# Kernel optimization log

Measured on AMD Instinct MI355X. Metric: run time of the kernel, lower is better.

## Reference

```python
import jax, jax.numpy as jnp
import numpy as np

B, S, D, H = 4, 2048, 768, 12
DEPTH = D // H


def setup_inputs() -> dict:
    key = jax.random.key(0)
    ks = jax.random.split(key, 8)
    scale = 1.0 / np.sqrt(D)
    inp = {
        "q": jax.random.normal(ks[0], (B, S, D), jnp.float32),
        "k": jax.random.normal(ks[1], (B, S, D), jnp.float32),
        "v": jax.random.normal(ks[2], (B, S, D), jnp.float32),
        # additive mask: 1.0 at disallowed (future) positions, causal
        "mask": jnp.triu(jnp.ones((S, S), jnp.float32), k=1)[None, None, :, :],
        "wq": jax.random.normal(ks[3], (D, D), jnp.float32) * scale,
        "wk": jax.random.normal(ks[4], (D, D), jnp.float32) * scale,
        "wv": jax.random.normal(ks[5], (D, D), jnp.float32) * scale,
        "w_dense": jax.random.normal(ks[6], (D, D), jnp.float32) * scale,
        "b_dense": jnp.zeros((D,), jnp.float32),
    }
    return inp


def _split_heads(x):
    b, s, _ = x.shape
    return x.reshape(b, s, H, DEPTH).transpose(0, 2, 1, 3)  # [B,H,S,depth]


def reference(q, k, v, mask, wq, wk, wv, w_dense, b_dense):
    qh = _split_heads(q @ wq.T)
    kh = _split_heads(k @ wk.T)
    vh = _split_heads(v @ wv.T)
    scale = jnp.sqrt(jnp.float32(DEPTH))
    logits = jnp.einsum("bhqd,bhkd->bhqk", qh, kh) / scale  # [B,H,S,S]
    logits = logits + mask * -1e9
    attn = jax.nn.softmax(logits, axis=-1)
    out = jnp.einsum("bhqk,bhkd->bhqd", attn, vh)
    out = out.transpose(0, 2, 1, 3).reshape(q.shape[0], -1, D)
    return out @ w_dense.T + b_dense
```

## Files before the change

kernel.cpp:

```cpp
#include <hip/hip_runtime.h>

typedef __attribute__((ext_vector_type(8))) short short8;
typedef __attribute__((ext_vector_type(4))) float f32x4;
typedef __attribute__((ext_vector_type(4))) unsigned int uint4v;

static __device__ __forceinline__ unsigned pack2(float x, float y) {
  unsigned ux = __float_as_uint(x) + 0x8000u;
  unsigned uy = __float_as_uint(y) + 0x8000u;
  return __builtin_amdgcn_perm(uy, ux, 0x07060302u);
}
static __device__ __forceinline__ unsigned packt(float x, float y) {
  return __builtin_amdgcn_perm(__float_as_uint(y), __float_as_uint(x), 0x07060302u);
}

#define GLDS(g, l)                                                                     \
  __builtin_amdgcn_global_load_lds((const __attribute__((address_space(1))) void*)(g), \
                                   (__attribute__((address_space(3))) void*)(l), 16, 0, 0)

__global__ __launch_bounds__(256) void cvt_all(const float* __restrict__ q,
                                               const float* __restrict__ k,
                                               const float* __restrict__ v,
                                               const float* __restrict__ w0,
                                               const float* __restrict__ w1,
                                               const float* __restrict__ w2,
                                               const float* __restrict__ w3,
                                               unsigned short* __restrict__ oq,
                                               unsigned short* __restrict__ ok,
                                               unsigned short* __restrict__ ov,
                                               unsigned short* __restrict__ o0,
                                               unsigned short* __restrict__ o1,
                                               unsigned short* __restrict__ o2,
                                               unsigned short* __restrict__ o3) {
  const int bx = blockIdx.x;
  const float* s;
  unsigned short* d;
  long i;
  if (bx < 18432) {
    int seg = bx / 6144;
    s = seg == 0 ? q : seg == 1 ? k : v;
    d = seg == 0 ? oq : seg == 1 ? ok : ov;
    i = (long)(bx - seg * 6144) * 256 + threadIdx.x;
  } else {
    int t = bx - 18432;
    int seg = t / 576;
    s = seg == 0 ? w0 : seg == 1 ? w1 : seg == 2 ? w2 : w3;
    d = seg == 0 ? o0 : seg == 1 ? o1 : seg == 2 ? o2 : o3;
    i = (long)(t - seg * 576) * 256 + threadIdx.x;
  }
  float4 val = ((const float4*)s)[i];
  uint2 o;
  o.x = pack2(val.x, val.y);
  o.y = pack2(val.z, val.w);
  *(uint2*)(d + 4 * i) = o;
}

template <int MODE>
static __device__ __forceinline__ void proj_body(const unsigned short* __restrict__ A,
                                                 const unsigned short* __restrict__ W,
                                                 unsigned short* __restrict__ O, int m0,
                                                 int n0, unsigned short* buf) {
  constexpr int K = 768;
  const int tid = threadIdx.x, lane = tid & 63, wave = tid >> 6;
  const int ln = lane & 15, quad = lane >> 4;
  const int wm = (wave & 1) << 6, wn = (wave >> 1) << 6;

  const int o0 = tid << 4, o1 = 4096 + (tid << 4);
  const unsigned short* gA0 = A + (long)(m0 + (o0 >> 6)) * K + ((o0 >> 4) & 3) * 8;
  const unsigned short* gA1 = A + (long)(m0 + (o1 >> 6)) * K + ((o1 >> 4) & 3) * 8;
  const unsigned short* gW0 = W + (long)(n0 + (o0 >> 6)) * K + ((o0 >> 4) & 3) * 8;
  const unsigned short* gW1 = W + (long)(n0 + (o1 >> 6)) * K + ((o1 >> 4) & 3) * 8;

  GLDS(gA0, buf + (o0 >> 1));
  GLDS(gA1, buf + (o1 >> 1));
  GLDS(gW0, buf + 8192 + (o0 >> 1));
  GLDS(gW1, buf + 8192 + (o1 >> 1));

  f32x4 acc[4][4] = {};
  for (int t = 0; t < 24; t++) {
    const int cur = t & 1, nxt = cur ^ 1;
    const int k1 = (t + 1) << 5;
    __syncthreads();
    if (t < 23) {
      GLDS(gA0 + k1, buf + nxt * 4096 + (o0 >> 1));
      GLDS(gA1 + k1, buf + nxt * 4096 + (o1 >> 1));
      GLDS(gW0 + k1, buf + 8192 + nxt * 4096 + (o0 >> 1));
      GLDS(gW1 + k1, buf + 8192 + nxt * 4096 + (o1 >> 1));
    }
    const unsigned short* As = buf + cur * 4096;
    const unsigned short* Bs = buf + 8192 + cur * 4096;
    short8 af[4], bfr[4];
#pragma unroll
    for (int mi = 0; mi < 4; mi++)
      af[mi] = *(const short8*)(As + (wm + mi * 16 + ln) * 32 + quad * 8);
#pragma unroll
    for (int ni = 0; ni < 4; ni++)
      bfr[ni] = *(const short8*)(Bs + (wn + ni * 16 + ln) * 32 + quad * 8);
#pragma unroll
    for (int mi = 0; mi < 4; mi++)
#pragma unroll
      for (int ni = 0; ni < 4; ni++)
        acc[mi][ni] = (MODE == 0)
                          ? __builtin_amdgcn_mfma_f32_16x16x32_bf16(bfr[ni], af[mi],
                                                                    acc[mi][ni], 0, 0, 0)
                          : __builtin_amdgcn_mfma_f32_16x16x32_bf16(af[mi], bfr[ni],
                                                                    acc[mi][ni], 0, 0, 0);
  }

  unsigned short* Ts = buf;
  __syncthreads();
  if (MODE == 0) {
#pragma unroll
    for (int mi = 0; mi < 4; mi++)
#pragma unroll
      for (int ni = 0; ni < 4; ni++) {
        f32x4 v = acc[mi][ni];
        int s = wm + mi * 16 + ln;
        int n = wn + ni * 16 + quad * 4;
        uint2 w2;
        w2.x = pack2(v[0], v[1]);
        w2.y = pack2(v[2], v[3]);
        *(uint2*)(Ts + s * 136 + n) = w2;
      }
    __syncthreads();
    const int part = tid & 7, sg0 = tid >> 3;
#pragma unroll
    for (int p = 0; p < 8; p++) {
      int seg = sg0 + p * 32;
      int hh = seg >> 7, s = seg & 127;
      short8 val = *(const short8*)(Ts + s * 136 + hh * 64 + part * 8);
      int gs = m0 + s;
      int bb = gs >> 11, srow = gs & 2047;
      int head = (n0 >> 6) + hh;
      *(short8*)(O + (((long)(bb * 12 + head) * 2048 + srow) << 6) + part * 8) = val;
    }
  } else {
#pragma unroll
    for (int mi = 0; mi < 4; mi++)
#pragma unroll
      for (int ni = 0; ni < 4; ni++) {
        f32x4 v = acc[mi][ni];
        int d = wn + ni * 16 + ln;
        int s = wm + mi * 16 + quad * 4;
        uint2 w2;
        w2.x = pack2(v[0], v[1]);
        w2.y = pack2(v[2], v[3]);
        *(uint2*)(Ts + d * 136 + s) = w2;
      }
    __syncthreads();
    const int part = tid & 15, r0 = tid >> 4;
    const int bb = m0 >> 11, sbase = m0 & 2047;
#pragma unroll
    for (int p = 0; p < 8; p++) {
      int d = r0 + p * 16;
      short8 val = *(const short8*)(Ts + d * 136 + part * 8);
      int head = (n0 >> 6) + (d >> 6);
      int dl = d & 63;
      *(short8*)(O + ((long)(bb * 12 + head) * 64 + dl) * 2048 + sbase + part * 8) = val;
    }
  }
}

__global__ __launch_bounds__(256) void proj_all(
    const unsigned short* __restrict__ qb, const unsigned short* __restrict__ kb,
    const unsigned short* __restrict__ vb, const unsigned short* __restrict__ wq,
    const unsigned short* __restrict__ wk, const unsigned short* __restrict__ wv,
    unsigned short* __restrict__ qh, unsigned short* __restrict__ kh,
    unsigned short* __restrict__ vt) {
  __shared__ unsigned short buf[17408];
  const int bx = blockIdx.x;
  const int xcd = bx & 7;
  const int i = bx >> 3;
  const int op = i / 48, j = i % 48;
  const int m0 = ((j / 6) * 8 + xcd) << 7, n0 = (j % 6) << 7;
  if (op == 0)
    proj_body<0>(qb, wq, qh, m0, n0, buf);
  else if (op == 1)
    proj_body<0>(kb, wk, kh, m0, n0, buf);
  else
    proj_body<1>(vb, wv, vt, m0, n0, buf);
}

__global__ __launch_bounds__(256) void dense_gemm(const unsigned short* __restrict__ A,
                                                  const unsigned short* __restrict__ W,
                                                  const float* __restrict__ bias,
                                                  float* __restrict__ out) {
  constexpr int K = 768;
  __shared__ unsigned short buf[16384];
  const int bx = blockIdx.x;
  const int xcd = bx & 7;
  const int i = bx >> 3;
  const int m0 = ((i / 6) * 8 + xcd) << 7;
  const int n0 = (i % 6) << 7;

  const int tid = threadIdx.x, lane = tid & 63, wave = tid >> 6;
  const int ln = lane & 15, quad = lane >> 4;
  const int wm = (wave & 1) << 6, wn = (wave >> 1) << 6;

  const int o0 = tid << 4, o1 = 4096 + (tid << 4);
  const unsigned short* gA0 = A + (long)(m0 + (o0 >> 6)) * K + ((o0 >> 4) & 3) * 8;
  const unsigned short* gA1 = A + (long)(m0 + (o1 >> 6)) * K + ((o1 >> 4) & 3) * 8;
  const unsigned short* gW0 = W + (long)(n0 + (o0 >> 6)) * K + ((o0 >> 4) & 3) * 8;
  const unsigned short* gW1 = W + (long)(n0 + (o1 >> 6)) * K + ((o1 >> 4) & 3) * 8;

  GLDS(gA0, buf + (o0 >> 1));
  GLDS(gA1, buf + (o1 >> 1));
  GLDS(gW0, buf + 8192 + (o0 >> 1));
  GLDS(gW1, buf + 8192 + (o1 >> 1));

  f32x4 acc[4][4] = {};
  for (int t = 0; t < 24; t++) {
    const int cur = t & 1, nxt = cur ^ 1;
    const int k1 = (t + 1) << 5;
    __syncthreads();
    if (t < 23) {
      GLDS(gA0 + k1, buf + nxt * 4096 + (o0 >> 1));
      GLDS(gA1 + k1, buf + nxt * 4096 + (o1 >> 1));
      GLDS(gW0 + k1, buf + 8192 + nxt * 4096 + (o0 >> 1));
      GLDS(gW1 + k1, buf + 8192 + nxt * 4096 + (o1 >> 1));
    }
    const unsigned short* As = buf + cur * 4096;
    const unsigned short* Bs = buf + 8192 + cur * 4096;
    short8 af[4], bfr[4];
#pragma unroll
    for (int mi = 0; mi < 4; mi++)
      af[mi] = *(const short8*)(As + (wm + mi * 16 + ln) * 32 + quad * 8);
#pragma unroll
    for (int ni = 0; ni < 4; ni++)
      bfr[ni] = *(const short8*)(Bs + (wn + ni * 16 + ln) * 32 + quad * 8);
#pragma unroll
    for (int mi = 0; mi < 4; mi++)
#pragma unroll
      for (int ni = 0; ni < 4; ni++)
        acc[mi][ni] =
            __builtin_amdgcn_mfma_f32_16x16x32_bf16(bfr[ni], af[mi], acc[mi][ni], 0, 0, 0);
  }

#pragma unroll
  for (int mi = 0; mi < 4; mi++) {
    const int m = m0 + wm + mi * 16 + ln;
#pragma unroll
    for (int ni = 0; ni < 4; ni++) {
      const int n = n0 + wn + ni * 16 + quad * 4;
      f32x4 v = acc[mi][ni];
      float4 bv = *(const float4*)(bias + n);
      float4 st;
      st.x = v[0] + bv.x;
      st.y = v[1] + bv.y;
      st.z = v[2] + bv.z;
      st.w = v[3] + bv.w;
      *(float4*)(out + (long)m * 768 + n) = st;
    }
  }
}

__global__ __launch_bounds__(256, 3) void attn_kernel(const unsigned short* __restrict__ Qh,
                                                      const unsigned short* __restrict__ Kh,
                                                      const unsigned short* __restrict__ Vt,
                                                      unsigned short* __restrict__ outp) {
  constexpr int S = 2048;
  constexpr float CEXP = 0.18033688011112042f;
  __shared__ unsigned short sbuf[16384];

  const int bx = blockIdx.x;
  const int xcd = bx & 7;
  const int ii = bx >> 3;
  const int pr = ii & 15, grp = ii >> 4;
  const int bh = grp * 8 + xcd;
  const int h = bh % 12, b = bh / 12;
  const int qtA = pr, qtB = 31 - pr;
  const int tid = threadIdx.x, wave = tid >> 6, lane = tid & 63;
  const int ln = lane & 15, quad = lane >> 4;

  const unsigned short* Qg = Qh + (long)(b * 12 + h) * S * 64;
  const unsigned short* Kg = Kh + (long)(b * 12 + h) * S * 64;
  const unsigned short* Vg = Vt + (long)(b * 12 + h) * 64 * S;

  const int qrA = qtA * 64 + wave * 16 + ln;
  const int qrB = qtB * 64 + wave * 16 + ln;

  short8 bQa0 = *(const short8*)(Qg + qrA * 64 + quad * 8);
  short8 bQa1 = *(const short8*)(Qg + qrA * 64 + 32 + quad * 8);
  short8 bQb0 = *(const short8*)(Qg + qrB * 64 + quad * 8);
  short8 bQb1 = *(const short8*)(Qg + qrB * 64 + 32 + quad * 8);

  float sumA = 0.f, sumB = 0.f;
  f32x4 Oa[4] = {};
  f32x4 Ob[4] = {};
  unsigned pkA[8][2], pkB[8][2];

  const int nkA = (qtA >> 1) + 1;
  const int nkB = (qtB >> 1) + 1;
  const int l0 = ln + ((quad & 1) << 5);
  const bool hi = quad >= 2;

  const int srow = tid >> 2, sc = (tid & 3) << 3;
  const int koff0 = srow * 64 + sc;
  const int koff1 = (srow + 64) * 64 + sc;
  const int koff2 = srow * 64 + 32 + sc;
  const int koff3 = (srow + 64) * 64 + 32 + sc;
  const long voff = (long)srow * 2048 + sc;

  short8 kc[4], vc[4];
  {
    kc[0] = *(const short8*)(Kg + koff0);
    kc[1] = *(const short8*)(Kg + koff1);
    kc[2] = *(const short8*)(Kg + koff2);
    kc[3] = *(const short8*)(Kg + koff3);
    vc[0] = *(const short8*)(Vg + voff);
    vc[1] = *(const short8*)(Vg + voff + 32);
    vc[2] = *(const short8*)(Vg + voff + 64);
    vc[3] = *(const short8*)(Vg + voff + 96);
  }

  for (int kt = 0; kt < nkB; kt++) {
    __syncthreads();
    {
      unsigned short* w = sbuf + tid * 8;
      *(short8*)(w) = kc[0];
      *(short8*)(w + 2048) = kc[1];
      *(short8*)(w + 4096) = kc[2];
      *(short8*)(w + 6144) = kc[3];
      *(short8*)(w + 8192) = vc[0];
      *(short8*)(w + 10240) = vc[1];
      *(short8*)(w + 12288) = vc[2];
      *(short8*)(w + 14336) = vc[3];
    }
    __syncthreads();
    if (kt + 1 < nkB) {
      const unsigned short* kg = Kg + (kt + 1) * 8192;
      const unsigned short* vg = Vg + (kt + 1) * 128;
      kc[0] = *(const short8*)(kg + koff0);
      kc[1] = *(const short8*)(kg + koff1);
      kc[2] = *(const short8*)(kg + koff2);
      kc[3] = *(const short8*)(kg + koff3);
      vc[0] = *(const short8*)(vg + voff);
      vc[1] = *(const short8*)(vg + voff + 32);
      vc[2] = *(const short8*)(vg + voff + 64);
      vc[3] = *(const short8*)(vg + voff + 96);
    }

    const bool actA = kt < nkA;
    const bool dgA = actA && (kt == nkA - 1);
    const bool dgB = (kt == nkB - 1);
    const int limA = actA ? (dgA ? ((qtA & 1) ? 8 : 4) : 8) : 0;
    const int limB = dgB ? ((qtB & 1) ? 8 : 4) : 8;
    const int limQ = limA > limB ? limA : limB;
    const int kbase = kt * 128 + quad * 4;

#pragma unroll
    for (int ni = 0; ni < 8; ni++) {
      if (ni < limQ) {
        const int fro = (ni * 16 + ln) * 32 + quad * 8;
        short8 k0 = *(const short8*)(sbuf + fro);
        short8 k1 = *(const short8*)(sbuf + 4096 + fro);
        const int key = kbase + ni * 16;
        if (ni < limA) {
          f32x4 s = {};
          s = __builtin_amdgcn_mfma_f32_16x16x32_bf16(k0, bQa0, s, 0, 0, 0);
          s = __builtin_amdgcn_mfma_f32_16x16x32_bf16(k1, bQa1, s, 0, 0, 0);
          float p0 = exp2f(s[0] * CEXP), p1 = exp2f(s[1] * CEXP);
          float p2 = exp2f(s[2] * CEXP), p3 = exp2f(s[3] * CEXP);
          if (dgA) {
            p0 = (key + 0 > qrA) ? 0.f : p0;
            p1 = (key + 1 > qrA) ? 0.f : p1;
            p2 = (key + 2 > qrA) ? 0.f : p2;
            p3 = (key + 3 > qrA) ? 0.f : p3;
          }
          sumA += (p0 + p1) + (p2 + p3);
          pkA[ni][0] = packt(p0, p1);
          pkA[ni][1] = packt(p2, p3);
        }
        if (ni < limB) {
          f32x4 s = {};
          s = __builtin_amdgcn_mfma_f32_16x16x32_bf16(k0, bQb0, s, 0, 0, 0);
          s = __builtin_amdgcn_mfma_f32_16x16x32_bf16(k1, bQb1, s, 0, 0, 0);
          float p0 = exp2f(s[0] * CEXP), p1 = exp2f(s[1] * CEXP);
          float p2 = exp2f(s[2] * CEXP), p3 = exp2f(s[3] * CEXP);
          if (dgB) {
            p0 = (key + 0 > qrB) ? 0.f : p0;
            p1 = (key + 1 > qrB) ? 0.f : p1;
            p2 = (key + 2 > qrB) ? 0.f : p2;
            p3 = (key + 3 > qrB) ? 0.f : p3;
          }
          sumB += (p0 + p1) + (p2 + p3);
          pkB[ni][0] = packt(p0, p1);
          pkB[ni][1] = packt(p2, p3);
        }
      }
    }

    auto mkB = [&](unsigned (&pk)[8][2], int kk) -> short8 {
      unsigned va0 = (unsigned)__shfl((int)pk[2 * kk][0], l0, 64);
      unsigned vb0 = (unsigned)__shfl((int)pk[2 * kk + 1][0], l0, 64);
      unsigned va1 = (unsigned)__shfl((int)pk[2 * kk][1], l0, 64);
      unsigned vb1 = (unsigned)__shfl((int)pk[2 * kk + 1][1], l0, 64);
      unsigned va2 = (unsigned)__shfl((int)pk[2 * kk][0], l0 + 16, 64);
      unsigned vb2 = (unsigned)__shfl((int)pk[2 * kk + 1][0], l0 + 16, 64);
      unsigned va3 = (unsigned)__shfl((int)pk[2 * kk][1], l0 + 16, 64);
      unsigned vb3 = (unsigned)__shfl((int)pk[2 * kk + 1][1], l0 + 16, 64);
      uint4v tv;
      tv.x = hi ? vb0 : va0;
      tv.y = hi ? vb1 : va1;
      tv.z = hi ? vb2 : va2;
      tv.w = hi ? vb3 : va3;
      return __builtin_bit_cast(short8, tv);
    };

    const int kkA = limA >> 1, kkB = limB >> 1;
#pragma unroll
    for (int kk = 0; kk < 4; kk++) {
      if (kk < kkB) {
        short8 Bb = mkB(pkB, kk);
        short8 Ba;
        if (kk < kkA) Ba = mkB(pkA, kk);
        const unsigned short* vp = sbuf + 8192 + kk * 2048;
#pragma unroll
        for (int di = 0; di < 4; di++) {
          short8 aV = *(const short8*)(vp + (di * 16 + ln) * 32 + quad * 8);
          Ob[di] = __builtin_amdgcn_mfma_f32_16x16x32_bf16(aV, Bb, Ob[di], 0, 0, 0);
          if (kk < kkA) Oa[di] = __builtin_amdgcn_mfma_f32_16x16x32_bf16(aV, Ba, Oa[di], 0, 0, 0);
        }
      }
    }
  }

  sumA += __shfl_xor(sumA, 16);
  sumA += __shfl_xor(sumA, 32);
  sumB += __shfl_xor(sumB, 16);
  sumB += __shfl_xor(sumB, 32);

  __syncthreads();
  unsigned short* Ts = sbuf;
  {
    float rlA = 1.0f / sumA, rlB = 1.0f / sumB;
    const int row = wave * 16 + ln;
#pragma unroll
    for (int di = 0; di < 4; di++) {
      uint2 wa, wb;
      wa.x = pack2(Oa[di][0] * rlA, Oa[di][1] * rlA);
      wa.y = pack2(Oa[di][2] * rlA, Oa[di][3] * rlA);
      wb.x = pack2(Ob[di][0] * rlB, Ob[di][1] * rlB);
      wb.y = pack2(Ob[di][2] * rlB, Ob[di][3] * rlB);
      *(uint2*)(Ts + row * 72 + di * 16 + quad * 4) = wa;
      *(uint2*)(Ts + (row + 64) * 72 + di * 16 + quad * 4) = wb;
    }
  }
  __syncthreads();
  const int part = tid & 7, r0 = tid >> 3;
#pragma unroll
  for (int p = 0; p < 4; p++) {
    int row = r0 + p * 32;
    int seg = row >> 6, qq = row & 63;
    int qrow = (seg ? qtB : qtA) * 64 + qq;
    short8 val = *(const short8*)(Ts + row * 72 + part * 8);
    *(short8*)(outp + ((long)b * S + qrow) * 768 + h * 64 + part * 8) = val;
  }
}

extern "C" void kernel_launch(void* const* d_in, const int* in_sizes, int n_in,
                              void* d_out, int out_size, void* d_ws, size_t ws_size,
                              hipStream_t stream) {
  const float* q = (const float*)d_in[0];
  const float* k = (const float*)d_in[1];
  const float* v = (const float*)d_in[2];
  const float* wq = (const float*)d_in[4];
  const float* wk = (const float*)d_in[5];
  const float* wv = (const float*)d_in[6];
  const float* wd = (const float*)d_in[7];
  const float* bd = (const float*)d_in[8];
  float* out = (float*)d_out;

  const long QKV = 4L * 2048 * 768;
  const long WN = 768L * 768;
  if (ws_size < (size_t)(7 * QKV + 4 * WN) * 2) return;

  unsigned short* qb = (unsigned short*)d_ws;
  unsigned short* kb = qb + QKV;
  unsigned short* vb = kb + QKV;
  unsigned short* wqb = vb + QKV;
  unsigned short* wkb = wqb + WN;
  unsigned short* wvb = wkb + WN;
  unsigned short* wdb = wvb + WN;
  unsigned short* qh = wdb + WN;
  unsigned short* kh = qh + QKV;
  unsigned short* vt = kh + QKV;
  unsigned short* at = vt + QKV;

  cvt_all<<<20736, 256, 0, stream>>>(q, k, v, wq, wk, wv, wd, qb, kb, vb, wqb, wkb, wvb, wdb);
  proj_all<<<1152, 256, 0, stream>>>(qb, kb, vb, wqb, wkb, wvb, qh, kh, vt);
  attn_kernel<<<768, 256, 0, stream>>>(qh, kh, vt, at);
  dense_gemm<<<384, 256, 0, stream>>>(at, wdb, bd, out);
}
```

Before: 271.2 us.

## Fuse fp32-to-bf16 activation conversion into projection GEMM and fold softmax scale into Q

The projection GEMM now streams the fp32 q/k/v activations straight into LDS with an XOR-swizzled layout and packs them to bf16 while loading fragments. This removes the separate conversion pass over the large activations and its bf16 round trip through global memory, leaving only a small weight-conversion kernel. The softmax exponent scale is applied to Q in the projection epilogue, so the attention inner loop drops a multiply per score. In exchange the A tile doubles in LDS size and global traffic, and each fragment load does extra packing ALU work.

```diff
diff --git a/kernel.cpp b/kernel.cpp
--- a/kernel.cpp
+++ b/kernel.cpp
@@ -17,36 +17,20 @@
   __builtin_amdgcn_global_load_lds((const __attribute__((address_space(1))) void*)(g), \
                                    (__attribute__((address_space(3))) void*)(l), 16, 0, 0)
 
-__global__ __launch_bounds__(256) void cvt_all(const float* __restrict__ q,
-                                               const float* __restrict__ k,
-                                               const float* __restrict__ v,
-                                               const float* __restrict__ w0,
-                                               const float* __restrict__ w1,
-                                               const float* __restrict__ w2,
-                                               const float* __restrict__ w3,
-                                               unsigned short* __restrict__ oq,
-                                               unsigned short* __restrict__ ok,
-                                               unsigned short* __restrict__ ov,
-                                               unsigned short* __restrict__ o0,
-                                               unsigned short* __restrict__ o1,
-                                               unsigned short* __restrict__ o2,
-                                               unsigned short* __restrict__ o3) {
-  const int bx = blockIdx.x;
-  const float* s;
-  unsigned short* d;
-  long i;
-  if (bx < 18432) {
-    int seg = bx / 6144;
-    s = seg == 0 ? q : seg == 1 ? k : v;
-    d = seg == 0 ? oq : seg == 1 ? ok : ov;
-    i = (long)(bx - seg * 6144) * 256 + threadIdx.x;
-  } else {
-    int t = bx - 18432;
-    int seg = t / 576;
-    s = seg == 0 ? w0 : seg == 1 ? w1 : seg == 2 ? w2 : w3;
-    d = seg == 0 ? o0 : seg == 1 ? o1 : seg == 2 ? o2 : o3;
-    i = (long)(t - seg * 576) * 256 + threadIdx.x;
-  }
+__global__ __launch_bounds__(256) void cvt_w(const float* __restrict__ w0,
+                                             const float* __restrict__ w1,
+                                             const float* __restrict__ w2,
+                                             const float* __restrict__ w3,
+                                             unsigned short* __restrict__ o0,
+                                             unsigned short* __restrict__ o1,
+                                             unsigned short* __restrict__ o2,
+                                             unsigned short* __restrict__ o3) {
+  int bx = blockIdx.x;
+  int seg = bx / 576;
+  int t = bx - seg * 576;
+  const float* s = seg == 0 ? w0 : seg == 1 ? w1 : seg == 2 ? w2 : w3;
+  unsigned short* d = seg == 0 ? o0 : seg == 1 ? o1 : seg == 2 ? o2 : o3;
+  long i = (long)t * 256 + threadIdx.x;
   float4 val = ((const float4*)s)[i];
   uint2 o;
   o.x = pack2(val.x, val.y);
@@ -55,25 +39,44 @@
 }
 
 template <int MODE>
-static __device__ __forceinline__ void proj_body(const unsigned short* __restrict__ A,
+static __device__ __forceinline__ void proj_body(const float* __restrict__ A,
                                                  const unsigned short* __restrict__ W,
                                                  unsigned short* __restrict__ O, int m0,
-                                                 int n0, unsigned short* buf) {
+                                                 int n0, unsigned short* buf, float scale) {
   constexpr int K = 768;
+  float* Af = (float*)buf;
+  unsigned short* Wb = buf + 16384;
   const int tid = threadIdx.x, lane = tid & 63, wave = tid >> 6;
   const int ln = lane & 15, quad = lane >> 4;
   const int wm = (wave & 1) << 6, wn = (wave >> 1) << 6;
 
+  const float* gA[4];
+  float* lA[4];
+#pragma unroll
+  for (int i = 0; i < 4; i++) {
+    int s = tid + i * 256;
+    int row = s >> 3;
+    int cg = (s & 7) ^ (row & 7);
+    gA[i] = A + (long)(m0 + row) * K + cg * 4;
+    lA[i] = Af + s * 4;
+  }
   const int o0 = tid << 4, o1 = 4096 + (tid << 4);
-  const unsigned short* gA0 = A + (long)(m0 + (o0 >> 6)) * K + ((o0 >> 4) & 3) * 8;
-  const unsigned short* gA1 = A + (long)(m0 + (o1 >> 6)) * K + ((o1 >> 4) & 3) * 8;
   const unsigned short* gW0 = W + (long)(n0 + (o0 >> 6)) * K + ((o0 >> 4) & 3) * 8;
   const unsigned short* gW1 = W + (long)(n0 + (o1 >> 6)) * K + ((o1 >> 4) & 3) * 8;
 
-  GLDS(gA0, buf + (o0 >> 1));
-  GLDS(gA1, buf + (o1 >> 1));
-  GLDS(gW0, buf + 8192 + (o0 >> 1));
-  GLDS(gW1, buf + 8192 + (o1 >> 1));
+  int fpo[4][2];
+#pragma unroll
+  for (int mi = 0; mi < 4; mi++) {
+    int R = wm + mi * 16 + ln;
+    int x = ln & 7;
+    fpo[mi][0] = (R * 8 + ((2 * quad) ^ x)) * 4;
+    fpo[mi][1] = (R * 8 + ((2 * quad + 1) ^ x)) * 4;
+  }
+
+#pragma unroll
+  for (int i = 0; i < 4; i++) GLDS(gA[i], lA[i]);
+  GLDS(gW0, Wb + (o0 >> 1));
+  GLDS(gW1, Wb + (o1 >> 1));
 
   f32x4 acc[4][4] = {};
   for (int t = 0; t < 24; t++) {
@@ -81,20 +84,28 @@
     const int k1 = (t + 1) << 5;
     __syncthreads();
     if (t < 23) {
-      GLDS(gA0 + k1, buf + nxt * 4096 + (o0 >> 1));
-      GLDS(gA1 + k1, buf + nxt * 4096 + (o1 >> 1));
-      GLDS(gW0 + k1, buf + 8192 + nxt * 4096 + (o0 >> 1));
-      GLDS(gW1 + k1, buf + 8192 + nxt * 4096 + (o1 >> 1));
-    }
-    const unsigned short* As = buf + cur * 4096;
-    const unsigned short* Bs = buf + 8192 + cur * 4096;
+#pragma unroll
+      for (int i = 0; i < 4; i++) GLDS(gA[i] + k1, lA[i] + nxt * 4096);
+      GLDS(gW0 + k1, Wb + nxt * 4096 + (o0 >> 1));
+      GLDS(gW1 + k1, Wb + nxt * 4096 + (o1 >> 1));
+    }
+    const float* Ac = Af + cur * 4096;
+    const unsigned short* Wc = Wb + cur * 4096;
     short8 af[4], bfr[4];
 #pragma unroll
-    for (int mi = 0; mi < 4; mi++)
-      af[mi] = *(const short8*)(As + (wm + mi * 16 + ln) * 32 + quad * 8);
+    for (int mi = 0; mi < 4; mi++) {
+      float4 fa = *(const float4*)(Ac + fpo[mi][0]);
+      float4 fb = *(const float4*)(Ac + fpo[mi][1]);
+      uint4v p;
+      p.x = pack2(fa.x, fa.y);
+      p.y = pack2(fa.z, fa.w);
+      p.z = pack2(fb.x, fb.y);
+      p.w = pack2(fb.z, fb.w);
+      af[mi] = __builtin_bit_cast(short8, p);
+    }
 #pragma unroll
     for (int ni = 0; ni < 4; ni++)
-      bfr[ni] = *(const short8*)(Bs + (wn + ni * 16 + ln) * 32 + quad * 8);
+      bfr[ni] = *(const short8*)(Wc + (wn + ni * 16 + ln) * 32 + quad * 8);
 #pragma unroll
     for (int mi = 0; mi < 4; mi++)
 #pragma unroll
@@ -117,8 +128,8 @@
         int s = wm + mi * 16 + ln;
         int n = wn + ni * 16 + quad * 4;
         uint2 w2;
-        w2.x = pack2(v[0], v[1]);
-        w2.y = pack2(v[2], v[3]);
+        w2.x = pack2(v[0] * scale, v[1] * scale);
+        w2.y = pack2(v[2] * scale, v[3] * scale);
         *(uint2*)(Ts + s * 136 + n) = w2;
       }
     __syncthreads();
@@ -161,23 +172,23 @@
 }
 
 __global__ __launch_bounds__(256) void proj_all(
-    const unsigned short* __restrict__ qb, const unsigned short* __restrict__ kb,
-    const unsigned short* __restrict__ vb, const unsigned short* __restrict__ wq,
-    const unsigned short* __restrict__ wk, const unsigned short* __restrict__ wv,
-    unsigned short* __restrict__ qh, unsigned short* __restrict__ kh,
-    unsigned short* __restrict__ vt) {
-  __shared__ unsigned short buf[17408];
+    const float* __restrict__ q, const float* __restrict__ k, const float* __restrict__ v,
+    const unsigned short* __restrict__ wq, const unsigned short* __restrict__ wk,
+    const unsigned short* __restrict__ wv, unsigned short* __restrict__ qh,
+    unsigned short* __restrict__ kh, unsigned short* __restrict__ vt) {
+  __shared__ __align__(16) unsigned short buf[24576];
   const int bx = blockIdx.x;
   const int xcd = bx & 7;
   const int i = bx >> 3;
   const int op = i / 48, j = i % 48;
   const int m0 = ((j / 6) * 8 + xcd) << 7, n0 = (j % 6) << 7;
+  constexpr float QSC = 0.18033688011112042f;
   if (op == 0)
-    proj_body<0>(qb, wq, qh, m0, n0, buf);
+    proj_body<0>(q, wq, qh, m0, n0, buf, QSC);
   else if (op == 1)
-    proj_body<0>(kb, wk, kh, m0, n0, buf);
+    proj_body<0>(k, wk, kh, m0, n0, buf, 1.0f);
   else
-    proj_body<1>(vb, wv, vt, m0, n0, buf);
+    proj_body<1>(v, wv, vt, m0, n0, buf, 1.0f);
 }
 
 __global__ __launch_bounds__(256) void dense_gemm(const unsigned short* __restrict__ A,
@@ -258,7 +269,6 @@
                                                       const unsigned short* __restrict__ Vt,
                                                       unsigned short* __restrict__ outp) {
   constexpr int S = 2048;
-  constexpr float CEXP = 0.18033688011112042f;
   __shared__ unsigned short sbuf[16384];
 
   const int bx = blockIdx.x;
@@ -358,8 +368,8 @@
           f32x4 s = {};
           s = __builtin_amdgcn_mfma_f32_16x16x32_bf16(k0, bQa0, s, 0, 0, 0);
           s = __builtin_amdgcn_mfma_f32_16x16x32_bf16(k1, bQa1, s, 0, 0, 0);
-          float p0 = exp2f(s[0] * CEXP), p1 = exp2f(s[1] * CEXP);
-          float p2 = exp2f(s[2] * CEXP), p3 = exp2f(s[3] * CEXP);
+          float p0 = exp2f(s[0]), p1 = exp2f(s[1]);
+          float p2 = exp2f(s[2]), p3 = exp2f(s[3]);
           if (dgA) {
             p0 = (key + 0 > qrA) ? 0.f : p0;
             p1 = (key + 1 > qrA) ? 0.f : p1;
@@ -374,8 +384,8 @@
           f32x4 s = {};
           s = __builtin_amdgcn_mfma_f32_16x16x32_bf16(k0, bQb0, s, 0, 0, 0);
           s = __builtin_amdgcn_mfma_f32_16x16x32_bf16(k1, bQb1, s, 0, 0, 0);
-          float p0 = exp2f(s[0] * CEXP), p1 = exp2f(s[1] * CEXP);
-          float p2 = exp2f(s[2] * CEXP), p3 = exp2f(s[3] * CEXP);
+          float p0 = exp2f(s[0]), p1 = exp2f(s[1]);
+          float p2 = exp2f(s[2]), p3 = exp2f(s[3]);
           if (dgB) {
             p0 = (key + 0 > qrB) ? 0.f : p0;
             p1 = (key + 1 > qrB) ? 0.f : p1;
@@ -472,12 +482,9 @@
 
   const long QKV = 4L * 2048 * 768;
   const long WN = 768L * 768;
-  if (ws_size < (size_t)(7 * QKV + 4 * WN) * 2) return;
-
-  unsigned short* qb = (unsigned short*)d_ws;
-  unsigned short* kb = qb + QKV;
-  unsigned short* vb = kb + QKV;
-  unsigned short* wqb = vb + QKV;
+  if (ws_size < (size_t)(4 * QKV + 4 * WN) * 2) return;
+
+  unsigned short* wqb = (unsigned short*)d_ws;
   unsigned short* wkb = wqb + WN;
   unsigned short* wvb = wkb + WN;
   unsigned short* wdb = wvb + WN;
@@ -486,8 +493,8 @@
   unsigned short* vt = kh + QKV;
   unsigned short* at = vt + QKV;
 
-  cvt_all<<<20736, 256, 0, stream>>>(q, k, v, wq, wk, wv, wd, qb, kb, vb, wqb, wkb, wvb, wdb);
-  proj_all<<<1152, 256, 0, stream>>>(qb, kb, vb, wqb, wkb, wvb, qh, kh, vt);
+  cvt_w<<<2304, 256, 0, stream>>>(wq, wk, wv, wd, wqb, wkb, wvb, wdb);
+  proj_all<<<1152, 256, 0, stream>>>(q, k, v, wqb, wkb, wvb, qh, kh, vt);
   attn_kernel<<<768, 256, 0, stream>>>(qh, kh, vt, at);
   dense_gemm<<<384, 256, 0, stream>>>(at, wdb, bd, out);
 }
```

Result: slower. 278.5 us (+2.7%).

## Fold softmax exp scale into Q projection and halve dense GEMM N-tile

Applied to the files above, without the earlier changes.

The softmax constant (log2(e)/sqrt(depth)) is now applied to the Q projection output before the bf16 pack, so the attention inner loop calls exp2f directly without a per-element multiply. Separately, the output dense GEMM uses 128x64 tiles instead of 128x128, doubling the grid to 768 blocks and shrinking LDS and the accumulator array, to fill more compute units on a small GEMM. Scaling Q before rounding to bf16 changes rounding slightly. Smaller tiles mean each A tile is reloaded once more.

```diff
diff --git a/kernel.cpp b/kernel.cpp
--- a/kernel.cpp
+++ b/kernel.cpp
@@ -58,7 +58,7 @@
 static __device__ __forceinline__ void proj_body(const unsigned short* __restrict__ A,
                                                  const unsigned short* __restrict__ W,
                                                  unsigned short* __restrict__ O, int m0,
-                                                 int n0, unsigned short* buf) {
+                                                 int n0, unsigned short* buf, float scale) {
   constexpr int K = 768;
   const int tid = threadIdx.x, lane = tid & 63, wave = tid >> 6;
   const int ln = lane & 15, quad = lane >> 4;
@@ -117,8 +117,8 @@
         int s = wm + mi * 16 + ln;
         int n = wn + ni * 16 + quad * 4;
         uint2 w2;
-        w2.x = pack2(v[0], v[1]);
-        w2.y = pack2(v[2], v[3]);
+        w2.x = pack2(v[0] * scale, v[1] * scale);
+        w2.y = pack2(v[2] * scale, v[3] * scale);
         *(uint2*)(Ts + s * 136 + n) = w2;
       }
     __syncthreads();
@@ -172,12 +172,13 @@
   const int i = bx >> 3;
   const int op = i / 48, j = i % 48;
   const int m0 = ((j / 6) * 8 + xcd) << 7, n0 = (j % 6) << 7;
+  constexpr float QSC = 0.18033688011112042f;
   if (op == 0)
-    proj_body<0>(qb, wq, qh, m0, n0, buf);
+    proj_body<0>(qb, wq, qh, m0, n0, buf, QSC);
   else if (op == 1)
-    proj_body<0>(kb, wk, kh, m0, n0, buf);
+    proj_body<0>(kb, wk, kh, m0, n0, buf, 1.0f);
   else
-    proj_body<1>(vb, wv, vt, m0, n0, buf);
+    proj_body<1>(vb, wv, vt, m0, n0, buf, 1.0f);
 }
 
 __global__ __launch_bounds__(256) void dense_gemm(const unsigned short* __restrict__ A,
@@ -185,29 +186,31 @@
                                                   const float* __restrict__ bias,
                                                   float* __restrict__ out) {
   constexpr int K = 768;
-  __shared__ unsigned short buf[16384];
+  __shared__ unsigned short buf[12288];
   const int bx = blockIdx.x;
   const int xcd = bx & 7;
-  const int i = bx >> 3;
-  const int m0 = ((i / 6) * 8 + xcd) << 7;
-  const int n0 = (i % 6) << 7;
+  const int rest = bx >> 3;
+  const int mgrp = rest / 12, nt = rest % 12;
+  const int m0 = (mgrp * 8 + xcd) << 7;
+  const int n0 = nt << 6;
 
   const int tid = threadIdx.x, lane = tid & 63, wave = tid >> 6;
   const int ln = lane & 15, quad = lane >> 4;
-  const int wm = (wave & 1) << 6, wn = (wave >> 1) << 6;
+  const int wm = (wave & 1) << 6, wn = (wave >> 1) << 5;
 
   const int o0 = tid << 4, o1 = 4096 + (tid << 4);
   const unsigned short* gA0 = A + (long)(m0 + (o0 >> 6)) * K + ((o0 >> 4) & 3) * 8;
   const unsigned short* gA1 = A + (long)(m0 + (o1 >> 6)) * K + ((o1 >> 4) & 3) * 8;
   const unsigned short* gW0 = W + (long)(n0 + (o0 >> 6)) * K + ((o0 >> 4) & 3) * 8;
-  const unsigned short* gW1 = W + (long)(n0 + (o1 >> 6)) * K + ((o1 >> 4) & 3) * 8;
-
-  GLDS(gA0, buf + (o0 >> 1));
-  GLDS(gA1, buf + (o1 >> 1));
-  GLDS(gW0, buf + 8192 + (o0 >> 1));
-  GLDS(gW1, buf + 8192 + (o1 >> 1));
-
-  f32x4 acc[4][4] = {};
+  unsigned short* lA0 = buf + (o0 >> 1);
+  unsigned short* lA1 = buf + (o1 >> 1);
+  unsigned short* lW0 = buf + 8192 + (o0 >> 1);
+
+  GLDS(gA0, lA0);
+  GLDS(gA1, lA1);
+  GLDS(gW0, lW0);
+
+  f32x4 acc[4][2] = {};
   for (int t = 0; t < 24; t++) {
     const int cur = t & 1, nxt = cur ^ 1;
     const int k1 = (t + 1) << 5;
@@ -215,22 +218,21 @@
     if (t < 23) {
       GLDS(gA0 + k1, buf + nxt * 4096 + (o0 >> 1));
       GLDS(gA1 + k1, buf + nxt * 4096 + (o1 >> 1));
-      GLDS(gW0 + k1, buf + 8192 + nxt * 4096 + (o0 >> 1));
-      GLDS(gW1 + k1, buf + 8192 + nxt * 4096 + (o1 >> 1));
+      GLDS(gW0 + k1, buf + 8192 + nxt * 2048 + (o0 >> 1));
     }
     const unsigned short* As = buf + cur * 4096;
-    const unsigned short* Bs = buf + 8192 + cur * 4096;
-    short8 af[4], bfr[4];
+    const unsigned short* Ws = buf + 8192 + cur * 2048;
+    short8 af[4], bfr[2];
 #pragma unroll
     for (int mi = 0; mi < 4; mi++)
       af[mi] = *(const short8*)(As + (wm + mi * 16 + ln) * 32 + quad * 8);
 #pragma unroll
-    for (int ni = 0; ni < 4; ni++)
-      bfr[ni] = *(const short8*)(Bs + (wn + ni * 16 + ln) * 32 + quad * 8);
-#pragma unroll
-    for (int mi = 0; mi < 4; mi++)
-#pragma unroll
-      for (int ni = 0; ni < 4; ni++)
+    for (int ni = 0; ni < 2; ni++)
+      bfr[ni] = *(const short8*)(Ws + (wn + ni * 16 + ln) * 32 + quad * 8);
+#pragma unroll
+    for (int mi = 0; mi < 4; mi++)
+#pragma unroll
+      for (int ni = 0; ni < 2; ni++)
         acc[mi][ni] =
             __builtin_amdgcn_mfma_f32_16x16x32_bf16(bfr[ni], af[mi], acc[mi][ni], 0, 0, 0);
   }
@@ -239,7 +241,7 @@
   for (int mi = 0; mi < 4; mi++) {
     const int m = m0 + wm + mi * 16 + ln;
 #pragma unroll
-    for (int ni = 0; ni < 4; ni++) {
+    for (int ni = 0; ni < 2; ni++) {
       const int n = n0 + wn + ni * 16 + quad * 4;
       f32x4 v = acc[mi][ni];
       float4 bv = *(const float4*)(bias + n);
@@ -258,7 +260,6 @@
                                                       const unsigned short* __restrict__ Vt,
                                                       unsigned short* __restrict__ outp) {
   constexpr int S = 2048;
-  constexpr float CEXP = 0.18033688011112042f;
   __shared__ unsigned short sbuf[16384];
 
   const int bx = blockIdx.x;
@@ -358,8 +359,8 @@
           f32x4 s = {};
           s = __builtin_amdgcn_mfma_f32_16x16x32_bf16(k0, bQa0, s, 0, 0, 0);
           s = __builtin_amdgcn_mfma_f32_16x16x32_bf16(k1, bQa1, s, 0, 0, 0);
-          float p0 = exp2f(s[0] * CEXP), p1 = exp2f(s[1] * CEXP);
-          float p2 = exp2f(s[2] * CEXP), p3 = exp2f(s[3] * CEXP);
+          float p0 = exp2f(s[0]), p1 = exp2f(s[1]);
+          float p2 = exp2f(s[2]), p3 = exp2f(s[3]);
           if (dgA) {
             p0 = (key + 0 > qrA) ? 0.f : p0;
             p1 = (key + 1 > qrA) ? 0.f : p1;
@@ -374,8 +375,8 @@
           f32x4 s = {};
           s = __builtin_amdgcn_mfma_f32_16x16x32_bf16(k0, bQb0, s, 0, 0, 0);
           s = __builtin_amdgcn_mfma_f32_16x16x32_bf16(k1, bQb1, s, 0, 0, 0);
-          float p0 = exp2f(s[0] * CEXP), p1 = exp2f(s[1] * CEXP);
-          float p2 = exp2f(s[2] * CEXP), p3 = exp2f(s[3] * CEXP);
+          float p0 = exp2f(s[0]), p1 = exp2f(s[1]);
+          float p2 = exp2f(s[2]), p3 = exp2f(s[3]);
           if (dgB) {
             p0 = (key + 0 > qrB) ? 0.f : p0;
             p1 = (key + 1 > qrB) ? 0.f : p1;
@@ -489,5 +490,5 @@
   cvt_all<<<20736, 256, 0, stream>>>(q, k, v, wq, wk, wv, wd, qb, kb, vb, wqb, wkb, wvb, wdb);
   proj_all<<<1152, 256, 0, stream>>>(qb, kb, vb, wqb, wkb, wvb, qh, kh, vt);
   attn_kernel<<<768, 256, 0, stream>>>(qh, kh, vt, at);
-  dense_gemm<<<384, 256, 0, stream>>>(at, wdb, bd, out);
-}
+  dense_gemm<<<768, 256, 0, stream>>>(at, wdb, bd, out);
+}
```

Result: no change. 275.2 us (+1.5%).
